# Kernel optimization log

Measured on AMD Instinct MI355X. Metric: run time of the kernel, lower is better.

The kernel has to match this reference:

```python
import jax, jax.numpy as jnp
import numpy as np

# ---- static config (mirrors MonitorRetina init) ----
N, S, H, W = 256, 1, 144, 256        # stimulus: [N, S, H, W]
HR, WR = 144, 256                    # retina height/width
FOV_HALF_RAD = 0.5 * 75.0 * np.pi / 180.0   # Angular retina, degrees=75
GELU_GAMMA = 1.7015043497085571      # variance-preserving gain for gelu
OUT_OF_RANGE = 10.0                  # grid value for rays missing the monitor


def isotropic_grid_2d(h, w):
    """Pixel-center coordinates, isotropic (normalized by max dim), [-1,1] on the long axis."""
    m = float(max(h, w))
    y = (jnp.arange(h, dtype=jnp.float32) * 2.0 + 1.0 - h) / m
    x = (jnp.arange(w, dtype=jnp.float32) * 2.0 + 1.0 - w) / m
    gy, gx = jnp.meshgrid(y, x, indexing="ij")
    return gx, gy  # each [h, w]


def rmat_3d(ax, ay, az):
    """Batched 3D rotation matrix R = Rz @ Ry @ Rx from Euler angles, each [N]."""
    cx, sx = jnp.cos(ax), jnp.sin(ax)
    cy, sy = jnp.cos(ay), jnp.sin(ay)
    cz, sz = jnp.cos(az), jnp.sin(az)
    one, zero = jnp.ones_like(ax), jnp.zeros_like(ax)
    Rx = jnp.stack([one, zero, zero, zero, cx, -sx, zero, sx, cx], -1).reshape(-1, 3, 3)
    Ry = jnp.stack([cy, zero, sy, zero, one, zero, -sy, zero, cy], -1).reshape(-1, 3, 3)
    Rz = jnp.stack([cz, -sz, zero, sz, cz, zero, zero, zero, one], -1).reshape(-1, 3, 3)
    return jnp.einsum("nij,njk,nkl->nil", Rz, Ry, Rx)  # [N,3,3]


def retina_rays(rmat):
    """Angular retina: pixel angles -> unit ray directions, rotated per batch. [N,HR,WR,3]."""
    gx, gy = isotropic_grid_2d(HR, WR)
    ax, ay = gx * FOV_HALF_RAD, gy * FOV_HALF_RAD
    a = jnp.sqrt(ax * ax + ay * ay) + 1e-12
    sinc = jnp.sin(a) / a
    d = jnp.stack([sinc * ax, sinc * ay, jnp.cos(a)], -1)  # [HR,WR,3]
    return jnp.einsum("nij,hwj->nhwi", rmat, d)


def monitor_project(rays):
    """Plane monitor at unit distance along +z: perspective divide to isotropic grid coords. [N,HR,WR,2]."""
    rz = rays[..., 2]
    safe = rz > 1e-3
    inv = jnp.where(safe, rz, 1.0)
    gx = jnp.where(safe, rays[..., 0] / inv, OUT_OF_RANGE)
    gy = jnp.where(safe, rays[..., 1] / inv, OUT_OF_RANGE)
    return jnp.stack([gx, gy], -1)


def isotropic_grid_sample_2d(x, grid, pad_value=0.0):
    """Bilinear sample x:[N,C,H,W] at grid:[N,H',W',2] (isotropic coords), constant padding."""
    m = float(max(H, W))
    px = (grid[..., 0] * m + W - 1.0) * 0.5  # [N,H',W'] pixel coords
    py = (grid[..., 1] * m + H - 1.0) * 0.5
    x0 = jnp.floor(px)
    y0 = jnp.floor(py)
    wx = px - x0
    wy = py - y0
    x0i = x0.astype(jnp.int32)
    y0i = y0.astype(jnp.int32)

    def corner(img, yi, xi):
        valid = (xi >= 0) & (xi < W) & (yi >= 0) & (yi < H)
        v = img[:, jnp.clip(yi, 0, H - 1), jnp.clip(xi, 0, W - 1)]  # [C,H',W']
        return jnp.where(valid[None], v, pad_value)

    def one(img, y0i, x0i, wx, wy):
        v00 = corner(img, y0i, x0i)
        v01 = corner(img, y0i, x0i + 1)
        v10 = corner(img, y0i + 1, x0i)
        v11 = corner(img, y0i + 1, x0i + 1)
        return (v00 * (1 - wx) + v01 * wx) * (1 - wy) + (v10 * (1 - wx) + v11 * wx) * wy

    return jax.vmap(one)(x, y0i, x0i, wx, wy)  # [N,C,H',W']


def setup_inputs() -> dict:
    key = jax.random.key(0)
    ks = jax.random.split(key, 8)
    F, D = 16, 128
    return {
        "stimulus": jax.random.normal(ks[0], (N, S, H, W), jnp.float32),
        "perspective": jax.random.normal(ks[1], (N, F), jnp.float32),
        "W1": jax.random.normal(ks[2], (F, D), jnp.float32) / np.sqrt(F),
        "b1": jnp.zeros((D,), jnp.float32),
        "W2": jax.random.normal(ks[3], (D, D), jnp.float32) / np.sqrt(D),
        "b2": jnp.zeros((D,), jnp.float32),
        "Wp": jax.random.normal(ks[4], (D, 3), jnp.float32) * 0.05,  # proj gains init near 0
        "bp": jnp.zeros((3,), jnp.float32),
    }


def reference(stimulus, perspective, W1, b1, W2, b2, Wp, bp):
    # MLP -> 3 angles -> rotation matrix (rmat)
    h = jax.nn.gelu(perspective @ W1 + b1) * GELU_GAMMA
    h = jax.nn.gelu(h @ W2 + b2) * GELU_GAMMA
    ang = h @ Wp + bp                      # [N,3]
    rm = rmat_3d(ang[:, 0], ang[:, 1], ang[:, 2])
    rays = retina_rays(rm)                 # [N,HR,WR,3]
    grid = monitor_project(rays)           # [N,HR,WR,2]
    # monitor_pixel / retina_pixel are Raw (identity) transforms
    return isotropic_grid_sample_2d(stimulus, grid, pad_value=0.0)  # [N,S,HR,WR]
```

## Files before the change

### kernel.cpp

```cpp
#include <hip/hip_runtime.h>
#include <math.h>

#define NB    256
#define IMG_H 144
#define IMG_W 256
#define IMG_ELEMS (IMG_H * IMG_W)
#define HR    144
#define WR    256
#define FDIM  16
#define DDIM  128

#define STRIDE 260
#define SIMG_FLOATS (147 * STRIDE + 4)

#define FOV_HALF_RAD 0.6544984694978736f
#define GELU_GAMMA   1.7015043497085571f
#define OUT_OF_RANGE 10.0f

typedef float f32x4 __attribute__((ext_vector_type(4)));
typedef const __attribute__((address_space(1))) unsigned int glb_u32;
typedef __attribute__((address_space(3))) unsigned int lds_u32;

__device__ __forceinline__ float gelu_gamma(float x) {
    const float k0 = 0.7978845608028654f;
    const float k1 = 0.044715f;
    float t = tanhf(k0 * (x + k1 * x * x * x));
    return 0.5f * x * (1.0f + t) * GELU_GAMMA;
}

__global__ void __launch_bounds__(1024, 4) fused_retina_kernel(
    const float* __restrict__ stim,
    const float* __restrict__ persp,
    const float* __restrict__ W1,
    const float* __restrict__ b1,
    const float* __restrict__ W2,
    const float* __restrict__ b2,
    const float* __restrict__ Wp,
    const float* __restrict__ bp,
    float* __restrict__ out)
{
    __shared__ float simg[SIMG_FLOATS];
    __shared__ float sh1[DDIM];
    __shared__ float sh2[DDIM];
    __shared__ float sAng[3];
    __shared__ float sR[9];

    const int tid  = threadIdx.x;
    const int n    = blockIdx.x;
    const int wid  = tid >> 6;
    const int lane = tid & 63;

    const float* __restrict__ img = stim + (size_t)n * IMG_ELEMS;

    if (tid < 340) {
        f32x4 z = {0.0f, 0.0f, 0.0f, 0.0f};
        int idx;
        if (tid < 195) {
            const int rr = tid / 65;
            const int g  = tid - rr * 65;
            const int s  = (rr == 0) ? 0 : (144 + rr);
            idx = s * STRIDE + g * 4;
        } else if (tid < 339) {
            idx = (tid - 194) * STRIDE;
        } else {
            idx = 147 * STRIDE;
        }
        *(f32x4*)&simg[idx] = z;
    }

    if (wid > 0) {
        const int v = wid - 1;
#pragma unroll
        for (int p = 0; p < 10; ++p) {
            const int r = v + 15 * p;
            if (r < IMG_H) {
                const float* gsrc = img + (size_t)r * IMG_W + lane * 4;
                float* ldst = &simg[(r + 1) * STRIDE + 4];
                __builtin_amdgcn_global_load_lds(
                    (glb_u32*)gsrc, (lds_u32*)ldst, 16, 0, 0);
            }
        }
    } else {
        float a0 = b1[lane], a1 = b1[lane + 64];
#pragma unroll
        for (int f = 0; f < FDIM; ++f) {
            const float p = persp[n * FDIM + f];
            a0 = fmaf(p, W1[f * DDIM + lane],      a0);
            a1 = fmaf(p, W1[f * DDIM + lane + 64], a1);
        }
        sh1[lane]      = gelu_gamma(a0);
        sh1[lane + 64] = gelu_gamma(a1);
        asm volatile("s_waitcnt lgkmcnt(0)" ::: "memory");

        float c0 = b2[lane], c1 = b2[lane + 64];
#pragma unroll 8
        for (int k = 0; k < DDIM; ++k) {
            const float s = sh1[k];
            c0 = fmaf(s, W2[k * DDIM + lane],      c0);
            c1 = fmaf(s, W2[k * DDIM + lane + 64], c1);
        }
        sh2[lane]      = gelu_gamma(c0);
        sh2[lane + 64] = gelu_gamma(c1);
        asm volatile("s_waitcnt lgkmcnt(0)" ::: "memory");

        if (lane < 3) {
            float a = bp[lane];
#pragma unroll 8
            for (int k = 0; k < DDIM; ++k)
                a = fmaf(sh2[k], Wp[k * 3 + lane], a);
            sAng[lane] = a;
        }
        asm volatile("s_waitcnt lgkmcnt(0)" ::: "memory");

        if (lane == 0) {
            const float cx = cosf(sAng[0]), sx = sinf(sAng[0]);
            const float cy = cosf(sAng[1]), sy = sinf(sAng[1]);
            const float cz = cosf(sAng[2]), sz = sinf(sAng[2]);
            sR[0] = cz * cy;  sR[1] = cz * sy * sx - sz * cx;  sR[2] = cz * sy * cx + sz * sx;
            sR[3] = sz * cy;  sR[4] = sz * sy * sx + cz * cx;  sR[5] = sz * sy * cx - cz * sx;
            sR[6] = -sy;      sR[7] = cy * sx;                 sR[8] = cy * cx;
        }
    }
    __syncthreads();

    const float r0 = sR[0], r1 = sR[1], r2 = sR[2];
    const float r3 = sR[3], r4 = sR[4], r5 = sR[5];
    const float r6 = sR[6], r7 = sR[7], r8 = sR[8];

    float* __restrict__ outn = out + (size_t)n * IMG_ELEMS;

    const int w     = tid & 255;
    const int hbase = tid >> 8;
    const float gx  = ((float)(2 * w + 1) - 256.0f) * (1.0f / 256.0f);
    const float axv = gx * FOV_HALF_RAD;
    const float ax2 = axv * axv;
    const float A0 = r0 * axv, A1 = r3 * axv, A2 = r6 * axv;

#pragma unroll 4
    for (int it = 0; it < 36; ++it) {
        const int h   = it * 4 + hbase;
        const int px0 = (h << 8) | w;

        const float gy  = ((float)(2 * h + 1) - 144.0f) * (1.0f / 256.0f);
        const float ayv = gy * FOV_HALF_RAD;
        const float tt  = fmaf(ayv, ayv, ax2);

        float sc = fmaf(tt, 2.7557319e-6f, -1.9841270e-4f);
        sc = fmaf(tt, sc,  8.3333333e-3f);
        sc = fmaf(tt, sc, -1.6666667e-1f);
        sc = fmaf(tt, sc,  1.0f);

        float ca = fmaf(tt, 2.4801587e-5f, -1.3888889e-3f);
        ca = fmaf(tt, ca,  4.1666667e-2f);
        ca = fmaf(tt, ca, -0.5f);
        ca = fmaf(tt, ca,  1.0f);

        const float rx = fmaf(sc, fmaf(r1, ayv, A0), r2 * ca);
        const float ry = fmaf(sc, fmaf(r4, ayv, A1), r5 * ca);
        const float rz = fmaf(sc, fmaf(r7, ayv, A2), r8 * ca);

        const float inv  = __builtin_amdgcn_rcpf(rz);
        const float s128 = 128.0f * inv;
        const bool  safe = rz > 0.001f;

        float pxf = fmaf(rx, s128, 127.5f);
        float pyf = fmaf(ry, s128, 71.5f);
        pxf = safe ? pxf : 300.0f;
        pyf = safe ? pyf : 300.0f;
        pxf = fminf(fmaxf(pxf, -1.0f), 256.0f);
        pyf = fminf(fmaxf(pyf, -1.0f), 144.0f);

        const float x0f = floorf(pxf), y0f = floorf(pyf);
        const float wx  = pxf - x0f,   wy  = pyf - y0f;
        const int   xi  = (int)x0f,    yi  = (int)y0f;

        const int a00 = yi * STRIDE + xi + (STRIDE + 4);
        const int a10 = a00 + STRIDE;

        const float v00 = simg[a00];
        const float v01 = simg[a00 + 1];
        const float v10 = simg[a10];
        const float v11 = simg[a10 + 1];

        const float top = fmaf(wx, v01 - v00, v00);
        const float bot = fmaf(wx, v11 - v10, v10);
        const float res = fmaf(wy, bot - top, top);

        __builtin_nontemporal_store(res, outn + px0);
    }
}

extern "C" void kernel_launch(void* const* d_in, const int* in_sizes, int n_in,
                              void* d_out, int out_size, void* d_ws, size_t ws_size,
                              hipStream_t stream) {
    const float* stimulus    = (const float*)d_in[0];
    const float* perspective = (const float*)d_in[1];
    const float* W1          = (const float*)d_in[2];
    const float* b1          = (const float*)d_in[3];
    const float* W2          = (const float*)d_in[4];
    const float* b2          = (const float*)d_in[5];
    const float* Wp          = (const float*)d_in[6];
    const float* bp          = (const float*)d_in[7];
    float* out = (float*)d_out;

    (void)d_ws; (void)ws_size;

    fused_retina_kernel<<<NB, 1024, 0, stream>>>(
        stimulus, perspective, W1, b1, W2, b2, Wp, bp, out);
}
```

Measured before the change: 114.3 us.

## Overlap sample-coordinate computation with async image staging into LDS

The single block-wide sync is split in two. A plain s_barrier now only publishes the rotation matrix, which the MLP wave has flushed with an lgkmcnt wait. Every thread then computes LDS addresses and bilinear weights for the first 18 rows while the global_load_lds image copies are still in flight. A full __syncthreads follows before those precomputed samples are gathered, so ray math overlaps the per-block image load latency. The cost is 54 extra live registers per thread at 1024 threads per block, which risks spills or lower occupancy.

```diff
diff --git a/kernel.cpp b/kernel.cpp
--- a/kernel.cpp
+++ b/kernel.cpp
@@ -15,7 +15,8 @@
 
 #define FOV_HALF_RAD 0.6544984694978736f
 #define GELU_GAMMA   1.7015043497085571f
-#define OUT_OF_RANGE 10.0f
+
+#define PRE 18
 
 typedef float f32x4 __attribute__((ext_vector_type(4)));
 typedef const __attribute__((address_space(1))) unsigned int glb_u32;
@@ -120,8 +121,10 @@
             sR[3] = sz * cy;  sR[4] = sz * sy * sx + cz * cx;  sR[5] = sz * sy * cx - cz * sx;
             sR[6] = -sy;      sR[7] = cy * sx;                 sR[8] = cy * cx;
         }
-    }
-    __syncthreads();
+        asm volatile("s_waitcnt lgkmcnt(0)" ::: "memory");
+    }
+
+    asm volatile("s_barrier" ::: "memory");
 
     const float r0 = sR[0], r1 = sR[1], r2 = sR[2];
     const float r3 = sR[3], r4 = sR[4], r5 = sR[5];
@@ -136,8 +139,71 @@
     const float ax2 = axv * axv;
     const float A0 = r0 * axv, A1 = r3 * axv, A2 = r6 * axv;
 
+    int   aA[PRE];
+    float wxA[PRE], wyA[PRE];
+#pragma unroll
+    for (int it = 0; it < PRE; ++it) {
+        const int h = it * 4 + hbase;
+
+        const float gy  = ((float)(2 * h + 1) - 144.0f) * (1.0f / 256.0f);
+        const float ayv = gy * FOV_HALF_RAD;
+        const float tt  = fmaf(ayv, ayv, ax2);
+
+        float sc = fmaf(tt, 2.7557319e-6f, -1.9841270e-4f);
+        sc = fmaf(tt, sc,  8.3333333e-3f);
+        sc = fmaf(tt, sc, -1.6666667e-1f);
+        sc = fmaf(tt, sc,  1.0f);
+
+        float ca = fmaf(tt, 2.4801587e-5f, -1.3888889e-3f);
+        ca = fmaf(tt, ca,  4.1666667e-2f);
+        ca = fmaf(tt, ca, -0.5f);
+        ca = fmaf(tt, ca,  1.0f);
+
+        const float rx = fmaf(sc, fmaf(r1, ayv, A0), r2 * ca);
+        const float ry = fmaf(sc, fmaf(r4, ayv, A1), r5 * ca);
+        const float rz = fmaf(sc, fmaf(r7, ayv, A2), r8 * ca);
+
+        const float inv  = __builtin_amdgcn_rcpf(rz);
+        const float s128 = 128.0f * inv;
+        const bool  safe = rz > 0.001f;
+
+        float pxf = fmaf(rx, s128, 127.5f);
+        float pyf = fmaf(ry, s128, 71.5f);
+        pxf = safe ? pxf : 300.0f;
+        pyf = safe ? pyf : 300.0f;
+        pxf = fminf(fmaxf(pxf, -1.0f), 256.0f);
+        pyf = fminf(fmaxf(pyf, -1.0f), 144.0f);
+
+        const float x0f = floorf(pxf), y0f = floorf(pyf);
+        wxA[it] = pxf - x0f;
+        wyA[it] = pyf - y0f;
+        const int xi = (int)x0f, yi = (int)y0f;
+        aA[it] = yi * STRIDE + xi + (STRIDE + 4);
+    }
+
+    __syncthreads();
+
+#pragma unroll
+    for (int it = 0; it < PRE; ++it) {
+        const int px0 = ((it * 4 + hbase) << 8) | w;
+        const int a00 = aA[it];
+        const int a10 = a00 + STRIDE;
+
+        const float v00 = simg[a00];
+        const float v01 = simg[a00 + 1];
+        const float v10 = simg[a10];
+        const float v11 = simg[a10 + 1];
+
+        const float wx = wxA[it], wy = wyA[it];
+        const float top = fmaf(wx, v01 - v00, v00);
+        const float bot = fmaf(wx, v11 - v10, v10);
+        const float res = fmaf(wy, bot - top, top);
+
+        __builtin_nontemporal_store(res, outn + px0);
+    }
+
 #pragma unroll 4
-    for (int it = 0; it < 36; ++it) {
+    for (int it = PRE; it < 36; ++it) {
         const int h   = it * 4 + hbase;
         const int px0 = (h << 8) | w;
 
```

Result: no change. 115.6 us (+1.1%).

## Split each image across two blocks by source-row half to halve LDS footprint

Applied to the files above, without the earlier changes.

Launches two blocks per image, each staging only half of the stimulus rows in LDS, and each writes only output pixels whose sample rows fall in its half. This reduces LDS per block so more blocks can be resident per CU and improves load parallelism. Both blocks redo the full ray computation and MLP, and many lanes do wasted sampling. The final projection is also replaced with a wave shuffle reduction.

```diff
diff --git a/kernel.cpp b/kernel.cpp
--- a/kernel.cpp
+++ b/kernel.cpp
@@ -5,17 +5,15 @@
 #define IMG_H 144
 #define IMG_W 256
 #define IMG_ELEMS (IMG_H * IMG_W)
-#define HR    144
-#define WR    256
 #define FDIM  16
 #define DDIM  128
 
 #define STRIDE 260
-#define SIMG_FLOATS (147 * STRIDE + 4)
+#define SROWS  76
+#define SIMG_FLOATS (SROWS * STRIDE)
 
 #define FOV_HALF_RAD 0.6544984694978736f
 #define GELU_GAMMA   1.7015043497085571f
-#define OUT_OF_RANGE 10.0f
 
 typedef float f32x4 __attribute__((ext_vector_type(4)));
 typedef const __attribute__((address_space(1))) unsigned int glb_u32;
@@ -28,7 +26,7 @@
     return 0.5f * x * (1.0f + t) * GELU_GAMMA;
 }
 
-__global__ void __launch_bounds__(1024, 4) fused_retina_kernel(
+__global__ void __launch_bounds__(1024, 8) fused_retina_kernel(
     const float* __restrict__ stim,
     const float* __restrict__ persp,
     const float* __restrict__ W1,
@@ -41,41 +39,46 @@
 {
     __shared__ float simg[SIMG_FLOATS];
     __shared__ float sh1[DDIM];
-    __shared__ float sh2[DDIM];
-    __shared__ float sAng[3];
     __shared__ float sR[9];
 
     const int tid  = threadIdx.x;
-    const int n    = blockIdx.x;
+    const int bid  = blockIdx.x;
+    const int n    = bid >> 1;
+    const int half = bid & 1;
     const int wid  = tid >> 6;
     const int lane = tid & 63;
 
     const float* __restrict__ img = stim + (size_t)n * IMG_ELEMS;
 
-    if (tid < 340) {
+    {
+        const int nzr = half ? 4 : 3;
         f32x4 z = {0.0f, 0.0f, 0.0f, 0.0f};
-        int idx;
-        if (tid < 195) {
-            const int rr = tid / 65;
-            const int g  = tid - rr * 65;
-            const int s  = (rr == 0) ? 0 : (144 + rr);
-            idx = s * STRIDE + g * 4;
-        } else if (tid < 339) {
-            idx = (tid - 194) * STRIDE;
+        if (tid < nzr * 65) {
+            const int zi = tid / 65;
+            const int g  = tid - zi * 65;
+            int row;
+            if (half) row = (zi == 0) ? 0 : (72 + zi);
+            else      row = (zi == 0) ? 0 : (73 + zi);
+            *(f32x4*)&simg[row * STRIDE + g * 4] = z;
         } else {
-            idx = 147 * STRIDE;
-        }
-        *(f32x4*)&simg[idx] = z;
+            const int t     = tid - nzr * 65;
+            const int nleft = half ? 72 : 73;
+            if (t < nleft)
+                *(f32x4*)&simg[(t + 1) * STRIDE] = z;
+        }
     }
+
+    const int row0  = half ? 72 : 0;
+    const int nrows = half ? 72 : 73;
 
     if (wid > 0) {
         const int v = wid - 1;
 #pragma unroll
-        for (int p = 0; p < 10; ++p) {
-            const int r = v + 15 * p;
-            if (r < IMG_H) {
-                const float* gsrc = img + (size_t)r * IMG_W + lane * 4;
-                float* ldst = &simg[(r + 1) * STRIDE + 4];
+        for (int p = 0; p < 5; ++p) {
+            const int j = v + 15 * p;
+            if (j < nrows) {
+                const float* gsrc = img + (size_t)(row0 + j) * IMG_W + lane * 4;
+                float* ldst = &simg[(j + 1) * STRIDE + 4];
                 __builtin_amdgcn_global_load_lds(
                     (glb_u32*)gsrc, (lds_u32*)ldst, 16, 0, 0);
             }
@@ -99,23 +102,24 @@
             c0 = fmaf(s, W2[k * DDIM + lane],      c0);
             c1 = fmaf(s, W2[k * DDIM + lane + 64], c1);
         }
-        sh2[lane]      = gelu_gamma(c0);
-        sh2[lane + 64] = gelu_gamma(c1);
-        asm volatile("s_waitcnt lgkmcnt(0)" ::: "memory");
-
-        if (lane < 3) {
-            float a = bp[lane];
-#pragma unroll 8
-            for (int k = 0; k < DDIM; ++k)
-                a = fmaf(sh2[k], Wp[k * 3 + lane], a);
-            sAng[lane] = a;
-        }
-        asm volatile("s_waitcnt lgkmcnt(0)" ::: "memory");
+        const float g0 = gelu_gamma(c0);
+        const float g1 = gelu_gamma(c1);
+
+        float p0 = fmaf(g0, Wp[lane * 3 + 0], g1 * Wp[(lane + 64) * 3 + 0]);
+        float p1 = fmaf(g0, Wp[lane * 3 + 1], g1 * Wp[(lane + 64) * 3 + 1]);
+        float p2 = fmaf(g0, Wp[lane * 3 + 2], g1 * Wp[(lane + 64) * 3 + 2]);
+#pragma unroll
+        for (int m = 32; m >= 1; m >>= 1) {
+            p0 += __shfl_xor(p0, m);
+            p1 += __shfl_xor(p1, m);
+            p2 += __shfl_xor(p2, m);
+        }
 
         if (lane == 0) {
-            const float cx = cosf(sAng[0]), sx = sinf(sAng[0]);
-            const float cy = cosf(sAng[1]), sy = sinf(sAng[1]);
-            const float cz = cosf(sAng[2]), sz = sinf(sAng[2]);
+            const float ax = p0 + bp[0], ay = p1 + bp[1], az = p2 + bp[2];
+            const float cx = cosf(ax), sx = sinf(ax);
+            const float cy = cosf(ay), sy = sinf(ay);
+            const float cz = cosf(az), sz = sinf(az);
             sR[0] = cz * cy;  sR[1] = cz * sy * sx - sz * cx;  sR[2] = cz * sy * cx + sz * sx;
             sR[3] = sz * cy;  sR[4] = sz * sy * sx + cz * cx;  sR[5] = sz * sy * cx - cz * sx;
             sR[6] = -sy;      sR[7] = cy * sx;                 sR[8] = cy * cx;
@@ -135,6 +139,7 @@
     const float axv = gx * FOV_HALF_RAD;
     const float ax2 = axv * axv;
     const float A0 = r0 * axv, A1 = r3 * axv, A2 = r6 * axv;
+    const int sb = half ? 71 : -1;
 
 #pragma unroll 4
     for (int it = 0; it < 36; ++it) {
@@ -174,8 +179,9 @@
         const float wx  = pxf - x0f,   wy  = pyf - y0f;
         const int   xi  = (int)x0f,    yi  = (int)y0f;
 
-        const int a00 = yi * STRIDE + xi + (STRIDE + 4);
-        const int a10 = a00 + STRIDE;
+        const bool mine = half ? (yi >= 72) : (yi <= 71);
+        const int  a00  = mine ? ((yi - sb) * STRIDE + xi + 4) : 4;
+        const int  a10  = a00 + STRIDE;
 
         const float v00 = simg[a00];
         const float v01 = simg[a00 + 1];
@@ -186,7 +192,8 @@
         const float bot = fmaf(wx, v11 - v10, v10);
         const float res = fmaf(wy, bot - top, top);
 
-        __builtin_nontemporal_store(res, outn + px0);
+        if (mine)
+            __builtin_nontemporal_store(res, outn + px0);
     }
 }
 
@@ -205,6 +212,6 @@
 
     (void)d_ws; (void)ws_size;
 
-    fused_retina_kernel<<<NB, 1024, 0, stream>>>(
+    fused_retina_kernel<<<NB * 2, 1024, 0, stream>>>(
         stimulus, perspective, W1, b1, W2, b2, Wp, bp, out);
 }
```

Measured after the change: 117.8 us. +3.1%, slower.
